# Performance work log

Measured on AMD Instinct MI355X. Metric: run time of the kernel, lower is better.

The kernel has to match this reference:

```python
import jax, jax.numpy as jnp
import numpy as np

B, T, E, D, N, L, NF = 4, 2048, 512, 512, 16, 4, 2048


def setup_inputs() -> dict:
    key = jax.random.key(0)
    ks = jax.random.split(key, 12)
    r = lambda k, s, sc=1.0: jax.random.normal(k, s, dtype=jnp.float32) * sc
    return {
        "text_emb": r(ks[0], (B, T, E)),
        "W_in": r(ks[1], (E, D), 1.0 / np.sqrt(E).astype(np.float32)),
        "b_in": jnp.zeros((D,), jnp.float32),
        "freq_pe": r(ks[2], (NF, D), 0.02),
        # diagonal-SSM (S4D) params per layer, stacked on leading L axis
        "A_log": r(ks[3], (L, D, N), 0.5),
        "B_ssm": r(ks[4], (L, D, N), 0.5),
        "C_ssm": r(ks[5], (L, D, N), 0.5),
        "log_dt": r(ks[6], (L, D), 0.5) - 4.6,  # dt ~ 0.01
        "D_skip": r(ks[7], (L, D), 0.5),
        "ln_f0_scale": jnp.ones((D,), jnp.float32),
        "ln_f0_bias": jnp.zeros((D,), jnp.float32),
        "W_f0": r(ks[8], (D, 1), 1.0 / np.sqrt(D).astype(np.float32)),
        "b_f0": jnp.zeros((1,), jnp.float32),
        "ln_en_scale": jnp.ones((D,), jnp.float32),
        "ln_en_bias": jnp.zeros((D,), jnp.float32),
        "W_en": r(ks[9], (D, 1), 1.0 / np.sqrt(D).astype(np.float32)),
        "b_en": jnp.zeros((1,), jnp.float32),
    }


def _layernorm(x, scale, bias, eps=1e-5):
    mu = jnp.mean(x, axis=-1, keepdims=True)
    var = jnp.mean(jnp.square(x - mu), axis=-1, keepdims=True)
    return (x - mu) * jax.lax.rsqrt(var + eps) * scale + bias


def _s4_layer(h, A_log, Bm, Cm, log_dt, Dsk):
    # h: [B, T, D]; diagonal SSM with ZOH discretization, scanned over T.
    dt = jnp.exp(log_dt)                 # [D]
    A = -jnp.exp(A_log)                  # [D, N], stable (negative real)
    Abar = jnp.exp(dt[:, None] * A)      # [D, N]
    Bbar = (Abar - 1.0) / A * Bm         # [D, N]
    u_t = jnp.transpose(h, (1, 0, 2))    # [T, B, D]
    x0 = jnp.zeros((h.shape[0], h.shape[2], A.shape[1]), h.dtype)  # [B, D, N]

    def step(x, u):
        x = Abar * x + Bbar * u[..., None]          # [B, D, N]
        y = jnp.einsum('bdn,dn->bd', x, Cm)         # readout
        return x, y

    _, ys = jax.lax.scan(step, x0, u_t)             # ys: [T, B, D]
    y = jnp.transpose(ys, (1, 0, 2)) + Dsk * h      # D skip connection
    return h + jax.nn.gelu(y)                       # residual + activation


def _forward(text_emb, W_in, b_in, freq_pe, A_log, B_ssm, C_ssm, log_dt,
             D_skip, ln_f0_scale, ln_f0_bias, W_f0, b_f0,
             ln_en_scale, ln_en_bias, W_en, b_en):
    x = text_emb @ W_in + b_in                      # [B, T, D]
    Tlen = x.shape[1]
    nf = freq_pe.shape[0]
    if nf >= Tlen:                                  # static-shape crop
        freq = freq_pe[:Tlen]
    else:                                           # static-shape edge pad
        pad = jnp.repeat(freq_pe[-1:], Tlen - nf, axis=0)
        freq = jnp.concatenate([freq_pe, pad], axis=0)
    h = x + freq[None, :, :]
    for l in range(A_log.shape[0]):
        h = _s4_layer(h, A_log[l], B_ssm[l], C_ssm[l], log_dt[l], D_skip[l])
    f0 = (_layernorm(h, ln_f0_scale, ln_f0_bias) @ W_f0 + b_f0)[..., 0]
    en = (_layernorm(h, ln_en_scale, ln_en_bias) @ W_en + b_en)[..., 0]
    return f0, en


def reference(text_emb, W_in, b_in, freq_pe, A_log, B_ssm, C_ssm, log_dt,
              D_skip, ln_f0_scale, ln_f0_bias, W_f0, b_f0,
              ln_en_scale, ln_en_bias, W_en, b_en):
    return _forward(text_emb, W_in, b_in, freq_pe, A_log, B_ssm, C_ssm,
                    log_dt, D_skip, ln_f0_scale, ln_f0_bias, W_f0, b_f0,
                    ln_en_scale, ln_en_bias, W_en, b_en)
```

## Files before the change

### kernel.cpp

```cpp
#include <hip/hip_runtime.h>

#define B_   4
#define T_   2048
#define E_   512
#define D_   512
#define N_   16
#define L_   4
#define TCH  32
#define ROWS_PB 4

typedef __bf16 bf16x8 __attribute__((ext_vector_type(8)));
typedef float  f32x4  __attribute__((ext_vector_type(4)));
typedef float  f32x2  __attribute__((ext_vector_type(2)));
typedef unsigned short us8 __attribute__((ext_vector_type(8)));

__device__ __forceinline__ float us2f(unsigned short u) {
    return __uint_as_float(((unsigned int)u) << 16);
}
__device__ __forceinline__ unsigned short f2us(float f) {
    unsigned int u = __float_as_uint(f);
    unsigned int r = (u + 0x7fffu + ((u >> 16) & 1u)) >> 16;
    return (unsigned short)r;
}
__device__ __forceinline__ float ldin(const void* p, int i, unsigned int f) {
    return f ? ((const float*)p)[i] : us2f(((const unsigned short*)p)[i]);
}
__device__ __forceinline__ unsigned int probe_f32(const void* lnfs) {
    return (((const unsigned int*)lnfs)[0] == 0x3F800000u) ? 1u : 0u;
}

#define PA    0
#define PB    32768
#define PC    65536
#define PDT   98304
#define PDSK  100352
#define PLFS  102400
#define PLFB  102912
#define PWF   103424
#define PLES  103936
#define PLEB  104448
#define PWEN  104960
#define PSC   105472
#define PRM_N 105474

__global__ __launch_bounds__(256) void prep_kernel(
    const void* X, const void* A_log, const void* B_ssm, const void* C_ssm,
    const void* log_dt, const void* D_skip,
    const void* lnfs, const void* lnfb, const void* Wf0,
    const void* lnes, const void* lneb, const void* Wen,
    const void* bf0, const void* ben,
    unsigned short* __restrict__ textc, float* __restrict__ P) {
    unsigned int f = probe_f32(lnfs);
    int bid = blockIdx.x;
    if (bid < 2048) {
        int i = (bid * 256 + threadIdx.x) * 8;
        if (f) {
            const float* xf = (const float*)X;
            us8 r;
#pragma unroll
            for (int j = 0; j < 8; j++) r[j] = f2us(xf[i + j]);
            *(us8*)(textc + i) = r;
        } else {
            *(us8*)(textc + i) = *(const us8*)((const unsigned short*)X + i);
        }
    } else {
        int i = (bid - 2048) * 256 + threadIdx.x;
        if      (i < PB)     P[i] = ldin(A_log,  i - PA,   f);
        else if (i < PC)     P[i] = ldin(B_ssm,  i - PB,   f);
        else if (i < PDT)    P[i] = ldin(C_ssm,  i - PC,   f);
        else if (i < PDSK)   P[i] = ldin(log_dt, i - PDT,  f);
        else if (i < PLFS)   P[i] = ldin(D_skip, i - PDSK, f);
        else if (i < PLFB)   P[i] = ldin(lnfs,   i - PLFS, f);
        else if (i < PWF)    P[i] = ldin(lnfb,   i - PLFB, f);
        else if (i < PLES)   P[i] = ldin(Wf0,    i - PWF,  f);
        else if (i < PLEB)   P[i] = ldin(lnes,   i - PLES, f);
        else if (i < PWEN)   P[i] = ldin(lneb,   i - PLEB, f);
        else if (i < PSC)    P[i] = ldin(Wen,    i - PWEN, f);
        else if (i == PSC)     P[i] = ldin(bf0, 0, f);
        else if (i == PSC + 1) P[i] = ldin(ben, 0, f);
    }
}

__global__ __launch_bounds__(256) void transpose_wt(const void* __restrict__ Win,
                                                    const void* __restrict__ lnfs,
                                                    unsigned short* __restrict__ Wt) {
    __shared__ float tile[64 * 65];
    unsigned int f = probe_f32(lnfs);
    int r = threadIdx.x >> 6, i = threadIdx.x & 63;
    int d0 = blockIdx.x * 64, e0 = blockIdx.y * 64;
#pragma unroll
    for (int k = 0; k < 16; k++) {
        int e = k * 4 + r;
        tile[e * 65 + i] = ldin(Win, (e0 + e) * D_ + d0 + i, f);
    }
    __syncthreads();
#pragma unroll
    for (int k = 0; k < 16; k++) {
        int dd = k * 4 + r;
        Wt[(size_t)(d0 + dd) * E_ + e0 + i] = f2us(tile[i * 65 + dd]);
    }
}

__global__ __launch_bounds__(256) void transpose_freq(const void* __restrict__ freq,
                                                      const void* __restrict__ b_in,
                                                      const void* __restrict__ lnfs,
                                                      float* __restrict__ freqT) {
    __shared__ float tile[64 * 65];
    unsigned int f = probe_f32(lnfs);
    int r = threadIdx.x >> 6, i = threadIdx.x & 63;
    int d0 = blockIdx.x * 64, t0 = blockIdx.y * 64;
#pragma unroll
    for (int k = 0; k < 16; k++) {
        int t = k * 4 + r;
        tile[t * 65 + i] = ldin(freq, (t0 + t) * D_ + d0 + i, f);
    }
    __syncthreads();
#pragma unroll
    for (int k = 0; k < 16; k++) {
        int dd = k * 4 + r;
        freqT[(size_t)(d0 + dd) * T_ + t0 + i] = tile[i * 65 + dd] + ldin(b_in, d0 + dd, f);
    }
}

__global__ __launch_bounds__(256) void gemm_kernel(const unsigned short* __restrict__ X,
                                                   const unsigned short* __restrict__ Wt,
                                                   const float* __restrict__ freqT,
                                                   float* __restrict__ H) {
    __shared__ unsigned short wlds[64 * 264];
    const int tid = threadIdx.x;
    const int w  = tid >> 6;
    const int ln = tid & 15;
    const int q  = (tid >> 4) & 3;
    const int d0 = blockIdx.x * 64;
    const int t0 = blockIdx.y * 128;
    const int b  = blockIdx.z;

    f32x4 acc[2][4];
#pragma unroll
    for (int i = 0; i < 2; i++)
#pragma unroll
        for (int j = 0; j < 4; j++) { acc[i][j][0]=0.f; acc[i][j][1]=0.f; acc[i][j][2]=0.f; acc[i][j][3]=0.f; }

    const size_t xbase = ((size_t)b * T_ + t0) * E_;

#pragma unroll
    for (int p = 0; p < 2; ++p) {
        if (p) __syncthreads();
#pragma unroll
        for (int it = 0; it < 8; ++it) {
            int flat = it * 256 + tid;
            int d = flat >> 5;
            int e = (flat & 31) << 3;
            bf16x8 v = *(const bf16x8*)(Wt + (size_t)(d0 + d) * E_ + p * 256 + e);
            *(bf16x8*)(wlds + d * 264 + e) = v;
        }
        __syncthreads();
#pragma unroll
        for (int s = 0; s < 8; ++s) {
            const int eo = s * 32 + q * 8;
            bf16x8 bfr[4];
#pragma unroll
            for (int j = 0; j < 4; j++)
                bfr[j] = *(const bf16x8*)(wlds + (j * 16 + ln) * 264 + eo);
#pragma unroll
            for (int sub = 0; sub < 2; ++sub) {
                const int t = w * 32 + sub * 16 + ln;
                bf16x8 afr = *(const bf16x8*)(X + xbase + (size_t)t * E_ + p * 256 + eo);
#pragma unroll
                for (int j = 0; j < 4; j++)
                    acc[sub][j] = __builtin_amdgcn_mfma_f32_16x16x32_bf16(afr, bfr[j], acc[sub][j], 0, 0, 0);
            }
        }
    }
#pragma unroll
    for (int sub = 0; sub < 2; ++sub) {
#pragma unroll
        for (int j = 0; j < 4; j++) {
            int d  = d0 + j * 16 + ln;
            int tb = t0 + w * 32 + sub * 16 + q * 4;
            f32x4 fr = *(const f32x4*)(freqT + (size_t)d * T_ + tb);
            f32x4 o  = acc[sub][j] + fr;
            *(f32x4*)(H + ((size_t)b * D_ + d) * T_ + tb) = o;
        }
    }
}

__global__ __launch_bounds__(256) void s4_kernel(float* __restrict__ H,
                                                 const float* __restrict__ P) {
    __shared__ float xl[ROWS_PB][64 * 33];
    const int w = threadIdx.x >> 6, lane = threadIdx.x & 63;
    const int row = blockIdx.x * ROWS_PB + w;
    const int d = row & (D_ - 1);
    float* Xw  = xl[w];
    float* Xme = Xw + lane * 33;
    float* gp  = H + (size_t)row * T_;

#pragma unroll
    for (int k = 0; k < 8; k++) {
        int idx = k * 256 + lane * 4;
        f32x4 v = *(const f32x4*)(gp + idx);
        int s = (idx >> 5) * 33 + (idx & 31);
        Xw[s] = v[0]; Xw[s + 1] = v[1]; Xw[s + 2] = v[2]; Xw[s + 3] = v[3];
    }
    __syncthreads();

    for (int l = 0; l < L_; ++l) {
        const int pb = (l * D_ + d) * N_;
        float dt  = __expf(P[PDT + l * D_ + d]);
        float Dsk = P[PDSK + l * D_ + d];
        f32x2 Ab[8], Bb[8];
#pragma unroll
        for (int n = 0; n < 8; n++) {
            float A0  = -__expf(P[PA + pb + 2 * n]);
            float A1  = -__expf(P[PA + pb + 2 * n + 1]);
            float ab0 = __expf(dt * A0), ab1 = __expf(dt * A1);
            Ab[n][0] = ab0; Ab[n][1] = ab1;
            Bb[n][0] = (ab0 - 1.f) / A0 * P[PB + pb + 2 * n];
            Bb[n][1] = (ab1 - 1.f) / A1 * P[PB + pb + 2 * n + 1];
        }
        f32x2 b[8];
#pragma unroll
        for (int n = 0; n < 8; n++) { b[n][0] = 0.f; b[n][1] = 0.f; }
#pragma unroll 4
        for (int j = 0; j < TCH; j++) {
            float uu = Xme[j];
            f32x2 u2; u2[0] = uu; u2[1] = uu;
#pragma unroll
            for (int n = 0; n < 8; n++) b[n] = Ab[n] * b[n] + Bb[n] * u2;
        }
        f32x2 M[8];
#pragma unroll
        for (int n = 0; n < 8; n++) {
            f32x2 m = Ab[n] * Ab[n];
            m = m * m; m = m * m; m = m * m;
            M[n] = m * m;
        }
#pragma unroll
        for (int dd = 1; dd < 64; dd <<= 1) {
            bool g = lane >= dd;
#pragma unroll
            for (int n = 0; n < 8; n++) {
                float bp0 = __shfl_up(b[n][0], (unsigned)dd, 64);
                float bp1 = __shfl_up(b[n][1], (unsigned)dd, 64);
                if (g) {
                    b[n][0] = fmaf(M[n][0], bp0, b[n][0]);
                    b[n][1] = fmaf(M[n][1], bp1, b[n][1]);
                }
            }
            if (dd < 32) {
#pragma unroll
                for (int n = 0; n < 8; n++) M[n] = M[n] * M[n];
            }
        }
        f32x2 x[8];
#pragma unroll
        for (int n = 0; n < 8; n++) {
            x[n][0] = __shfl_up(b[n][0], 1u, 64);
            x[n][1] = __shfl_up(b[n][1], 1u, 64);
            if (lane == 0) { x[n][0] = 0.f; x[n][1] = 0.f; }
        }
        f32x2 Cc[8];
#pragma unroll
        for (int n = 0; n < 8; n++) { Cc[n][0] = P[PC + pb + 2 * n]; Cc[n][1] = P[PC + pb + 2 * n + 1]; }
#pragma unroll 4
        for (int j = 0; j < TCH; j++) {
            float uu = Xme[j];
            f32x2 u2; u2[0] = uu; u2[1] = uu;
#pragma unroll
            for (int n = 0; n < 8; n++) x[n] = Ab[n] * x[n] + Bb[n] * u2;
            f32x2 ya; ya[0] = 0.f; ya[1] = 0.f;
            f32x2 yb; yb[0] = 0.f; yb[1] = 0.f;
#pragma unroll
            for (int n = 0; n < 8; n += 2) {
                ya = x[n] * Cc[n] + ya;
                yb = x[n + 1] * Cc[n + 1] + yb;
            }
            float y = (ya[0] + ya[1]) + (yb[0] + yb[1]);
            y = fmaf(Dsk, uu, y);
            float y3  = y * y * y;
            float zin = 0.7978845608028654f * fmaf(0.044715f, y3, y);
            float e2  = __expf(2.f * zin);
            float th  = 1.f - 2.f / (e2 + 1.f);
            Xme[j] = fmaf(0.5f * y, th, fmaf(0.5f, y, uu));
        }
    }
    __syncthreads();
#pragma unroll
    for (int k = 0; k < 8; k++) {
        int idx = k * 256 + lane * 4;
        int s = (idx >> 5) * 33 + (idx & 31);
        f32x4 v; v[0] = Xw[s]; v[1] = Xw[s + 1]; v[2] = Xw[s + 2]; v[3] = Xw[s + 3];
        *(f32x4*)(gp + idx) = v;
    }
}

__global__ __launch_bounds__(256) void final_kernel(const float* __restrict__ H,
                                                    const float* __restrict__ P,
                                                    void* __restrict__ out,
                                                    const void* __restrict__ lnfs_raw) {
    __shared__ float red[4][8][64];
    unsigned int f = probe_f32(lnfs_raw);
    int tid = threadIdx.x;
    int w = tid >> 6, tl = tid & 63;
    int tg = blockIdx.x * 64 + tl;
    int b = tg >> 11, t = tg & (T_ - 1);
    float S1=0.f,S2=0.f,Pf=0.f,Pe=0.f,Cf=0.f,Ce=0.f,Df=0.f,De=0.f;
    const float* hp = H + ((size_t)b * D_) * T_ + t;
#pragma unroll 4
    for (int i = 0; i < 128; i++) {
        int d = w * 128 + i;
        float hv = hp[(size_t)d * T_];
        float sf = P[PLFS + d], bfv = P[PLFB + d], wf = P[PWF + d];
        float se = P[PLES + d], bev = P[PLEB + d], we = P[PWEN + d];
        S1 += hv; S2 = fmaf(hv, hv, S2);
        float tf = sf * wf, te = se * we;
        Pf = fmaf(hv, tf, Pf); Pe = fmaf(hv, te, Pe);
        Cf += tf; Ce += te;
        Df = fmaf(bfv, wf, Df); De = fmaf(bev, we, De);
    }
    red[w][0][tl]=S1; red[w][1][tl]=S2; red[w][2][tl]=Pf; red[w][3][tl]=Pe;
    red[w][4][tl]=Cf; red[w][5][tl]=Ce; red[w][6][tl]=Df; red[w][7][tl]=De;
    __syncthreads();
    if (w == 0) {
        float a[8];
#pragma unroll
        for (int k = 0; k < 8; k++)
            a[k] = red[0][k][tl] + red[1][k][tl] + red[2][k][tl] + red[3][k][tl];
        float mu  = a[0] * (1.f / 512.f);
        float var = a[1] * (1.f / 512.f) - mu * mu;
        float r   = rsqrtf(var + 1e-5f);
        float f0  = r * (a[2] - mu * a[4]) + a[6] + P[PSC + 0];
        float en  = r * (a[3] - mu * a[5]) + a[7] + P[PSC + 1];
        if (f) {
            ((float*)out)[tg]           = f0;
            ((float*)out)[B_ * T_ + tg] = en;
        } else {
            ((unsigned short*)out)[tg]           = f2us(f0);
            ((unsigned short*)out)[B_ * T_ + tg] = f2us(en);
        }
    }
}

extern "C" void kernel_launch(void* const* d_in, const int* in_sizes, int n_in,
                              void* d_out, int out_size, void* d_ws, size_t ws_size,
                              hipStream_t stream) {
    (void)in_sizes; (void)n_in; (void)out_size; (void)ws_size;
    float* ws = (float*)d_ws;
    float* P     = ws;
    float* H     = ws + 105504;
    float* freqT = ws + 4299808;
    unsigned short* textc = (unsigned short*)(ws + 5348384);
    unsigned short* Wt    = (unsigned short*)(ws + 7445536);

    prep_kernel<<<dim3(2048 + (PRM_N + 255) / 256), dim3(256), 0, stream>>>(
        d_in[0], d_in[4], d_in[5], d_in[6], d_in[7], d_in[8],
        d_in[9], d_in[10], d_in[11], d_in[13], d_in[14], d_in[15],
        d_in[12], d_in[16], textc, P);
    transpose_wt  <<<dim3(8, 8),  dim3(256), 0, stream>>>(d_in[1], d_in[9], Wt);
    transpose_freq<<<dim3(8, 32), dim3(256), 0, stream>>>(d_in[3], d_in[2], d_in[9], freqT);
    gemm_kernel<<<dim3(8, 16, 4), dim3(256), 0, stream>>>(textc, Wt, freqT, H);
    s4_kernel<<<dim3(512), dim3(256), 0, stream>>>(H, P);
    final_kernel<<<dim3(128), dim3(256), 0, stream>>>(H, P, d_out, d_in[9]);
}
```

Baseline: 198.3 us.

## Fold weight transpose into prep kernel and read freq directly in GEMM epilogue

Merges the W_in transpose into the prep kernel as extra blocks and removes the separate freq transpose kernel. The GEMM epilogue now reads freq_pe and b_in directly with strided scalar loads, which drops two launches and the freqT round trip through the workspace. The cost is uncoalesced epilogue loads in the GEMM. The S4 kernel also gets a launch-bounds occupancy hint, and its C coefficients are now loaded at the start of each layer, which raises register pressure.

```diff
diff --git a/kernel.cpp b/kernel.cpp
--- a/kernel.cpp
+++ b/kernel.cpp
@@ -43,16 +43,23 @@
 #define PSC   105472
 #define PRM_N 105474
 
+#define NB_TEXT 2048
+#define NB_PRM  413
+#define NB_WT   64
+
 __global__ __launch_bounds__(256) void prep_kernel(
-    const void* X, const void* A_log, const void* B_ssm, const void* C_ssm,
+    const void* X, const void* Win,
+    const void* A_log, const void* B_ssm, const void* C_ssm,
     const void* log_dt, const void* D_skip,
     const void* lnfs, const void* lnfb, const void* Wf0,
     const void* lnes, const void* lneb, const void* Wen,
     const void* bf0, const void* ben,
-    unsigned short* __restrict__ textc, float* __restrict__ P) {
+    unsigned short* __restrict__ textc, unsigned short* __restrict__ Wt,
+    float* __restrict__ P) {
+    __shared__ float tile[64 * 65];
     unsigned int f = probe_f32(lnfs);
     int bid = blockIdx.x;
-    if (bid < 2048) {
+    if (bid < NB_TEXT) {
         int i = (bid * 256 + threadIdx.x) * 8;
         if (f) {
             const float* xf = (const float*)X;
@@ -63,8 +70,8 @@
         } else {
             *(us8*)(textc + i) = *(const us8*)((const unsigned short*)X + i);
         }
-    } else {
-        int i = (bid - 2048) * 256 + threadIdx.x;
+    } else if (bid < NB_TEXT + NB_PRM) {
+        int i = (bid - NB_TEXT) * 256 + threadIdx.x;
         if      (i < PB)     P[i] = ldin(A_log,  i - PA,   f);
         else if (i < PC)     P[i] = ldin(B_ssm,  i - PB,   f);
         else if (i < PDT)    P[i] = ldin(C_ssm,  i - PC,   f);
@@ -78,55 +85,32 @@
         else if (i < PSC)    P[i] = ldin(Wen,    i - PWEN, f);
         else if (i == PSC)     P[i] = ldin(bf0, 0, f);
         else if (i == PSC + 1) P[i] = ldin(ben, 0, f);
-    }
-}
-
-__global__ __launch_bounds__(256) void transpose_wt(const void* __restrict__ Win,
-                                                    const void* __restrict__ lnfs,
-                                                    unsigned short* __restrict__ Wt) {
-    __shared__ float tile[64 * 65];
-    unsigned int f = probe_f32(lnfs);
-    int r = threadIdx.x >> 6, i = threadIdx.x & 63;
-    int d0 = blockIdx.x * 64, e0 = blockIdx.y * 64;
-#pragma unroll
-    for (int k = 0; k < 16; k++) {
-        int e = k * 4 + r;
-        tile[e * 65 + i] = ldin(Win, (e0 + e) * D_ + d0 + i, f);
-    }
-    __syncthreads();
-#pragma unroll
-    for (int k = 0; k < 16; k++) {
-        int dd = k * 4 + r;
-        Wt[(size_t)(d0 + dd) * E_ + e0 + i] = f2us(tile[i * 65 + dd]);
-    }
-}
-
-__global__ __launch_bounds__(256) void transpose_freq(const void* __restrict__ freq,
-                                                      const void* __restrict__ b_in,
-                                                      const void* __restrict__ lnfs,
-                                                      float* __restrict__ freqT) {
-    __shared__ float tile[64 * 65];
-    unsigned int f = probe_f32(lnfs);
-    int r = threadIdx.x >> 6, i = threadIdx.x & 63;
-    int d0 = blockIdx.x * 64, t0 = blockIdx.y * 64;
-#pragma unroll
-    for (int k = 0; k < 16; k++) {
-        int t = k * 4 + r;
-        tile[t * 65 + i] = ldin(freq, (t0 + t) * D_ + d0 + i, f);
-    }
-    __syncthreads();
-#pragma unroll
-    for (int k = 0; k < 16; k++) {
-        int dd = k * 4 + r;
-        freqT[(size_t)(d0 + dd) * T_ + t0 + i] = tile[i * 65 + dd] + ldin(b_in, d0 + dd, f);
+    } else {
+        int tb = bid - (NB_TEXT + NB_PRM);
+        int d0 = (tb >> 3) * 64, e0 = (tb & 7) * 64;
+        int r = threadIdx.x >> 6, i = threadIdx.x & 63;
+#pragma unroll
+        for (int k = 0; k < 16; k++) {
+            int e = k * 4 + r;
+            tile[e * 65 + i] = ldin(Win, (e0 + e) * D_ + d0 + i, f);
+        }
+        __syncthreads();
+#pragma unroll
+        for (int k = 0; k < 16; k++) {
+            int dd = k * 4 + r;
+            Wt[(size_t)(d0 + dd) * E_ + e0 + i] = f2us(tile[i * 65 + dd]);
+        }
     }
 }
 
 __global__ __launch_bounds__(256) void gemm_kernel(const unsigned short* __restrict__ X,
                                                    const unsigned short* __restrict__ Wt,
-                                                   const float* __restrict__ freqT,
+                                                   const void* __restrict__ freq,
+                                                   const void* __restrict__ b_in,
+                                                   const void* __restrict__ lnfs,
                                                    float* __restrict__ H) {
     __shared__ unsigned short wlds[64 * 264];
+    const unsigned int fl = probe_f32(lnfs);
     const int tid = threadIdx.x;
     const int w  = tid >> 6;
     const int ln = tid & 15;
@@ -178,15 +162,18 @@
         for (int j = 0; j < 4; j++) {
             int d  = d0 + j * 16 + ln;
             int tb = t0 + w * 32 + sub * 16 + q * 4;
-            f32x4 fr = *(const f32x4*)(freqT + (size_t)d * T_ + tb);
-            f32x4 o  = acc[sub][j] + fr;
+            float bi = ldin(b_in, d, fl);
+            f32x4 o;
+#pragma unroll
+            for (int r4 = 0; r4 < 4; r4++)
+                o[r4] = acc[sub][j][r4] + ldin(freq, (tb + r4) * D_ + d, fl) + bi;
             *(f32x4*)(H + ((size_t)b * D_ + d) * T_ + tb) = o;
         }
     }
 }
 
-__global__ __launch_bounds__(256) void s4_kernel(float* __restrict__ H,
-                                                 const float* __restrict__ P) {
+__global__ __launch_bounds__(256, 2) void s4_kernel(float* __restrict__ H,
+                                                    const float* __restrict__ P) {
     __shared__ float xl[ROWS_PB][64 * 33];
     const int w = threadIdx.x >> 6, lane = threadIdx.x & 63;
     const int row = blockIdx.x * ROWS_PB + w;
@@ -208,7 +195,7 @@
         const int pb = (l * D_ + d) * N_;
         float dt  = __expf(P[PDT + l * D_ + d]);
         float Dsk = P[PDSK + l * D_ + d];
-        f32x2 Ab[8], Bb[8];
+        f32x2 Ab[8], Bb[8], Cc[8];
 #pragma unroll
         for (int n = 0; n < 8; n++) {
             float A0  = -__expf(P[PA + pb + 2 * n]);
@@ -217,6 +204,8 @@
             Ab[n][0] = ab0; Ab[n][1] = ab1;
             Bb[n][0] = (ab0 - 1.f) / A0 * P[PB + pb + 2 * n];
             Bb[n][1] = (ab1 - 1.f) / A1 * P[PB + pb + 2 * n + 1];
+            Cc[n][0] = P[PC + pb + 2 * n];
+            Cc[n][1] = P[PC + pb + 2 * n + 1];
         }
         f32x2 b[8];
 #pragma unroll
@@ -259,9 +248,6 @@
             x[n][1] = __shfl_up(b[n][1], 1u, 64);
             if (lane == 0) { x[n][0] = 0.f; x[n][1] = 0.f; }
         }
-        f32x2 Cc[8];
-#pragma unroll
-        for (int n = 0; n < 8; n++) { Cc[n][0] = P[PC + pb + 2 * n]; Cc[n][1] = P[PC + pb + 2 * n + 1]; }
 #pragma unroll 4
         for (int j = 0; j < TCH; j++) {
             float uu = Xme[j];
@@ -348,17 +334,14 @@
     float* ws = (float*)d_ws;
     float* P     = ws;
     float* H     = ws + 105504;
-    float* freqT = ws + 4299808;
-    unsigned short* textc = (unsigned short*)(ws + 5348384);
-    unsigned short* Wt    = (unsigned short*)(ws + 7445536);
-
-    prep_kernel<<<dim3(2048 + (PRM_N + 255) / 256), dim3(256), 0, stream>>>(
-        d_in[0], d_in[4], d_in[5], d_in[6], d_in[7], d_in[8],
+    unsigned short* textc = (unsigned short*)(ws + 4299808);
+    unsigned short* Wt    = (unsigned short*)(ws + 6396960);
+
+    prep_kernel<<<dim3(NB_TEXT + NB_PRM + NB_WT), dim3(256), 0, stream>>>(
+        d_in[0], d_in[1], d_in[4], d_in[5], d_in[6], d_in[7], d_in[8],
         d_in[9], d_in[10], d_in[11], d_in[13], d_in[14], d_in[15],
-        d_in[12], d_in[16], textc, P);
-    transpose_wt  <<<dim3(8, 8),  dim3(256), 0, stream>>>(d_in[1], d_in[9], Wt);
-    transpose_freq<<<dim3(8, 32), dim3(256), 0, stream>>>(d_in[3], d_in[2], d_in[9], freqT);
-    gemm_kernel<<<dim3(8, 16, 4), dim3(256), 0, stream>>>(textc, Wt, freqT, H);
+        d_in[12], d_in[16], textc, Wt, P);
+    gemm_kernel<<<dim3(8, 16, 4), dim3(256), 0, stream>>>(textc, Wt, d_in[3], d_in[2], d_in[9], H);
     s4_kernel<<<dim3(512), dim3(256), 0, stream>>>(H, P);
     final_kernel<<<dim3(128), dim3(256), 0, stream>>>(H, P, d_out, d_in[9]);
 }
```

Result: faster. 187.6 us (-5.4%).
